# Kernel optimization log

Measured on AMD Instinct MI355X. Metric: run time of the kernel, lower is better.

## Reference

```python
import jax, jax.numpy as jnp
import numpy as np

N_NODES = 50000
IN_CH = 512
HID = 256
HEADS = 4
N_LAYERS = 2
LN_EPS = 1e-5


def _layer_norm(x, g, b):
    mu = jnp.mean(x, axis=-1, keepdims=True)
    var = jnp.mean((x - mu) ** 2, axis=-1, keepdims=True)
    return (x - mu) * jax.lax.rsqrt(var + LN_EPS) * g + b


def _trans_conv(x, wq, bq, wk, bk, wv, bv):
    # x: [N, HID]; projections -> [N, HEADS, HID]
    N = x.shape[0]
    qs = (x @ wq + bq).reshape(N, HEADS, HID)
    ks = (x @ wk + bk).reshape(N, HEADS, HID)
    vs = (x @ wv + bv).reshape(N, HEADS, HID)
    # NOTE: global Frobenius norm, matching torch.norm(t, p=2)
    qs = qs / jnp.linalg.norm(qs)
    ks = ks / jnp.linalg.norm(ks)
    kvs = jnp.einsum('lhm,lhd->hmd', ks, vs)                 # [H, C, C]
    attn_num = jnp.einsum('nhm,hmd->nhd', qs, kvs) + N * vs  # [N, H, C]
    ks_sum = jnp.sum(ks, axis=0)                             # [H, C]
    denom = jnp.einsum('nhm,hm->nh', qs, ks_sum)[..., None] + N
    return jnp.mean(attn_num / denom, axis=1)                # [N, HID]


def setup_inputs() -> dict:
    key = jax.random.key(0)
    ks = jax.random.split(key, 32)
    s_in = 1.0 / np.sqrt(IN_CH)
    s_h = 1.0 / np.sqrt(HID)
    inp = {
        'x': jax.random.normal(ks[0], (N_NODES, IN_CH), jnp.float32),
        'fc_w': jax.random.uniform(ks[1], (IN_CH, HID), jnp.float32, -s_in, s_in),
        'fc_b': jax.random.uniform(ks[2], (HID,), jnp.float32, -s_in, s_in),
        'ln0_g': jnp.ones((HID,), jnp.float32),
        'ln0_b': jnp.zeros((HID,), jnp.float32),
    }
    for i in range(N_LAYERS):
        base = 3 + i * 8
        inp[f'wq{i}'] = jax.random.uniform(ks[base + 0], (HID, HID * HEADS), jnp.float32, -s_h, s_h)
        inp[f'bq{i}'] = jax.random.uniform(ks[base + 1], (HID * HEADS,), jnp.float32, -s_h, s_h)
        inp[f'wk{i}'] = jax.random.uniform(ks[base + 2], (HID, HID * HEADS), jnp.float32, -s_h, s_h)
        inp[f'bk{i}'] = jax.random.uniform(ks[base + 3], (HID * HEADS,), jnp.float32, -s_h, s_h)
        inp[f'wv{i}'] = jax.random.uniform(ks[base + 4], (HID, HID * HEADS), jnp.float32, -s_h, s_h)
        inp[f'bv{i}'] = jax.random.uniform(ks[base + 5], (HID * HEADS,), jnp.float32, -s_h, s_h)
        inp[f'ln{i + 1}_g'] = jnp.ones((HID,), jnp.float32)
        inp[f'ln{i + 1}_b'] = jnp.zeros((HID,), jnp.float32)
    return inp


def reference(x, fc_w, fc_b, ln0_g, ln0_b,
              wq0, bq0, wk0, bk0, wv0, bv0, ln1_g, ln1_b,
              wq1, bq1, wk1, bk1, wv1, bv1, ln2_g, ln2_b):
    # input FFN path (ffn is hard-coded True); dropout is identity in eval mode
    h = jax.nn.relu(_layer_norm(x @ fc_w + fc_b, ln0_g, ln0_b))
    layers = [(wq0, bq0, wk0, bk0, wv0, bv0, ln1_g, ln1_b),
              (wq1, bq1, wk1, bk1, wv1, bv1, ln2_g, ln2_b)]
    for (wq, bq, wk, bk, wv, bv, g, b) in layers:
        prev = h
        h = _trans_conv(h, wq, bq, wk, bk, wv, bv)
        h = (h + prev) / 2.0
        h = jax.nn.relu(_layer_norm(h, g, b))
    return h
```

## Files before the change

kernel.cpp:

```cpp
#include <hip/hip_runtime.h>

#define NN    50000
#define IN_CH 512
#define HID   256
#define PJ    1024
#define FN    50000.0f
#define KTP   50176
#define NCH   98
#define CHK   512

typedef __attribute__((ext_vector_type(4)))  float f32x4;
typedef __attribute__((ext_vector_type(16))) float f32x16;
typedef __attribute__((ext_vector_type(4)))  int   i32x4;
typedef __attribute__((ext_vector_type(8)))  unsigned short u16x8;

__device__ inline void mfma16(f32x4& c, i32x4 a, i32x4 b){
  asm("v_mfma_f32_16x16x32_bf16 %0, %1, %2, %0" : "+v"(c) : "v"(a), "v"(b));
}
__device__ inline void mfma32(f32x16& c, i32x4 a, i32x4 b){
  asm("v_mfma_f32_32x32x16_bf16 %0, %1, %2, %0" : "+v"(c) : "v"(a), "v"(b));
}

__device__ inline unsigned short f2bf(float f){
  unsigned int u = __builtin_bit_cast(unsigned int, f);
  unsigned int r = (u + 0x7fffu + ((u >> 16) & 1u)) >> 16;
  return (unsigned short)r;
}
__device__ inline float bf2f(unsigned short u){
  unsigned int x = ((unsigned int)u) << 16;
  return __builtin_bit_cast(float, x);
}

__device__ inline float wave_reduce(float v){
  #pragma unroll
  for(int o=32;o>0;o>>=1) v += __shfl_down(v,o,64);
  return v;
}
__device__ inline float block_reduce(float v, float* sh4){
  v = wave_reduce(v);
  int lane = threadIdx.x & 63, wv = threadIdx.x >> 6;
  if(lane==0) sh4[wv] = v;
  __syncthreads();
  float r = sh4[0]+sh4[1]+sh4[2]+sh4[3];
  __syncthreads();
  return r;
}

__global__ void wconv(const float* __restrict__ w, unsigned short* __restrict__ wt){
  int idx = blockIdx.x*256 + threadIdx.x;
  if(idx >= IN_CH*HID) return;
  int k = idx >> 8, n = idx & 255;
  wt[((size_t)(k>>6)*256 + n)*64 + (k&63)] = f2bf(w[idx]);
}

__global__ __launch_bounds__(512)
void ffn_gemm(const float* __restrict__ X, const unsigned short* __restrict__ FWT2,
              const float* __restrict__ bias, const float* __restrict__ g,
              const float* __restrict__ b2, unsigned short* __restrict__ hbo){
  __shared__ __align__(16) unsigned char smem[55296];
  unsigned short (*as)[72] = (unsigned short(*)[72])smem;
  unsigned short (*bs)[72] = (unsigned short(*)[72])(smem + 18432);
  int t = threadIdx.x;
  int bm = blockIdx.x*128;
  int w = t>>6, lane = t&63;
  int wr = w>>2, wc = w&3;
  f32x4 acc[4][4];
  #pragma unroll
  for(int i=0;i<4;i++)
    #pragma unroll
    for(int j=0;j<4;j++) acc[i][j] = (f32x4){0.f,0.f,0.f,0.f};

  for(int k0=0;k0<IN_CH;k0+=64){
    { int r = t>>2, q = t&3;
      const float* src = X + (size_t)(bm+r)*IN_CH + k0 + q*16;
      bool ok = (bm+r) < NN;
      #pragma unroll
      for(int i=0;i<4;i++){
        float4 v = ok ? *(const float4*)(src + i*4) : make_float4(0.f,0.f,0.f,0.f);
        ushort4 u; u.x=f2bf(v.x); u.y=f2bf(v.y); u.z=f2bf(v.z); u.w=f2bf(v.w);
        *(ushort4*)&as[r][q*16 + i*4] = u;
      }
    }
    { int n = t>>1, q = t&1;
      const unsigned short* src = FWT2 + (size_t)(k0>>6)*16384 + (size_t)t*32;
      #pragma unroll
      for(int i=0;i<4;i++)
        *(u16x8*)&bs[n][q*32 + i*8] = *(const u16x8*)(src + i*8);
    }
    __syncthreads();
    #pragma unroll
    for(int ks=0;ks<2;ks++){
      i32x4 af[4], bfv[4];
      #pragma unroll
      for(int i=0;i<4;i++) af[i]  = *(const i32x4*)&as[wr*64 + i*16 + (lane&15)][ks*32 + (lane>>4)*8];
      #pragma unroll
      for(int j=0;j<4;j++) bfv[j] = *(const i32x4*)&bs[wc*64 + j*16 + (lane&15)][ks*32 + (lane>>4)*8];
      #pragma unroll
      for(int i=0;i<4;i++)
        #pragma unroll
        for(int j=0;j<4;j++) mfma16(acc[i][j], af[i], bfv[j]);
    }
    __syncthreads();
  }
  int cb = wc*64;
  #pragma unroll
  for(int j=0;j<4;j++){
    float bb = bias[cb + j*16 + (lane&15)];
    #pragma unroll
    for(int i=0;i<4;i++)
      #pragma unroll
      for(int r=0;r<4;r++) acc[i][j][r] += bb;
  }
  float (*lnp)[4][2] = (float(*)[4][2])smem;
  float (*lnstat)[2] = (float(*)[2])(smem + 4096);
  #pragma unroll
  for(int i=0;i<4;i++)
    #pragma unroll
    for(int r=0;r<4;r++){
      float s=0.f, q=0.f;
      #pragma unroll
      for(int j=0;j<4;j++){ float a=acc[i][j][r]; s+=a; q+=a*a; }
      #pragma unroll
      for(int m=1;m<16;m<<=1){ s += __shfl_xor(s,m,64); q += __shfl_xor(q,m,64); }
      if((lane&15)==0){
        int row = wr*64 + i*16 + (lane>>4)*4 + r;
        lnp[row][wc][0]=s; lnp[row][wc][1]=q;
      }
    }
  __syncthreads();
  if(t<128){
    float s=0.f,q=0.f;
    #pragma unroll
    for(int c=0;c<4;c++){ s+=lnp[t][c][0]; q+=lnp[t][c][1]; }
    float mu = s*(1.f/HID);
    float var = q*(1.f/HID) - mu*mu;
    lnstat[t][0]=mu; lnstat[t][1]=rsqrtf(var+1e-5f);
  }
  __syncthreads();
  #pragma unroll
  for(int j=0;j<4;j++){
    int col = cb + j*16 + (lane&15);
    float gg = g[col], bb = b2[col];
    #pragma unroll
    for(int i=0;i<4;i++)
      #pragma unroll
      for(int r=0;r<4;r++){
        int row = wr*64 + i*16 + (lane>>4)*4 + r;
        int grow = bm + row;
        if(grow<NN){
          float y = fmaxf((acc[i][j][r]-lnstat[row][0])*lnstat[row][1]*gg + bb, 0.f);
          hbo[(size_t)grow*HID + col] = f2bf(y);
        }
      }
  }
}

__global__ void ln_relu2(const float* __restrict__ in, const float* __restrict__ g,
                         const float* __restrict__ b, unsigned short* __restrict__ outb,
                         float* __restrict__ outf, int M){
  int lane = threadIdx.x & 63, wv = threadIdx.x >> 6;
  int row = blockIdx.x*4 + wv;
  if(row>=M) return;
  const float* r = in + (size_t)row*HID;
  float v[4], sum=0.f, sq=0.f;
  #pragma unroll
  for(int j=0;j<4;j++){ v[j]=r[lane+j*64]; sum+=v[j]; sq+=v[j]*v[j]; }
  sum = wave_reduce(sum); sq = wave_reduce(sq);
  sum = __shfl(sum,0,64); sq = __shfl(sq,0,64);
  float mu = sum*(1.f/HID);
  float var = sq*(1.f/HID) - mu*mu;
  float rs = rsqrtf(var + 1e-5f);
  #pragma unroll
  for(int j=0;j<4;j++){ int c=lane+j*64;
    float y = fmaxf((v[j]-mu)*rs*g[c] + b[c], 0.f);
    if(outb) outb[(size_t)row*HID + c] = f2bf(y);
    if(outf) outf[(size_t)row*HID + c] = y;
  }
}

__global__ __launch_bounds__(256)
void transpose_h(const unsigned short* __restrict__ hb, unsigned short* __restrict__ ht){
  __shared__ unsigned short ts[64][72];
  int r0 = blockIdx.x*64, c0 = blockIdx.y*64;
  int t = threadIdx.x;
  { int r = t&63, q = t>>6;
    #pragma unroll
    for(int i=0;i<2;i++){
      int c = q*16 + i*8;
      u16x8 v = {0,0,0,0,0,0,0,0};
      if(r0+r < NN) v = *(const u16x8*)(hb + (size_t)(r0+r)*HID + c0 + c);
      *(u16x8*)&ts[r][c] = v;
    }
  }
  __syncthreads();
  { int c = t>>2, q = t&3;
    unsigned short tmp[16];
    #pragma unroll
    for(int i=0;i<16;i++) tmp[i] = ts[q*16+i][c];
    unsigned short* dst = ht + (size_t)(c0+c)*KTP + r0 + q*16;
    *(u16x8*)(dst)   = *(u16x8*)&tmp[0];
    *(u16x8*)(dst+8) = *(u16x8*)&tmp[8];
  }
}

__global__ __launch_bounds__(256)
void gram_mfma(const unsigned short* __restrict__ ht, float* __restrict__ gp){
  __shared__ unsigned short as[128][72], bs[128][72];
  int q = blockIdx.x, ch = blockIdx.y;
  int r0 = (q>>1)*128, c0 = (q&1)*128;
  int t = threadIdx.x, w=t>>6, lane=t&63;
  int wr=w>>1, wc=w&1;
  f32x4 acc[4][4];
  #pragma unroll
  for(int i=0;i<4;i++)
    #pragma unroll
    for(int j=0;j<4;j++) acc[i][j] = (f32x4){0.f,0.f,0.f,0.f};
  size_t kbase = (size_t)ch*CHK;
  for(int k0=0;k0<CHK;k0+=64){
    { int r = t>>1, h2 = t&1;
      const unsigned short* srcA = ht + (size_t)(r0+r)*KTP + kbase + k0 + h2*32;
      const unsigned short* srcB = ht + (size_t)(c0+r)*KTP + kbase + k0 + h2*32;
      #pragma unroll
      for(int i=0;i<4;i++) *(u16x8*)&as[r][h2*32+i*8] = *(const u16x8*)(srcA + i*8);
      #pragma unroll
      for(int i=0;i<4;i++) *(u16x8*)&bs[r][h2*32+i*8] = *(const u16x8*)(srcB + i*8);
    }
    __syncthreads();
    #pragma unroll
    for(int ks=0;ks<2;ks++){
      i32x4 af[4], bfv[4];
      #pragma unroll
      for(int i=0;i<4;i++) af[i]  = *(const i32x4*)&as[wr*64 + i*16 + (lane&15)][ks*32 + (lane>>4)*8];
      #pragma unroll
      for(int j=0;j<4;j++) bfv[j] = *(const i32x4*)&bs[wc*64 + j*16 + (lane&15)][ks*32 + (lane>>4)*8];
      #pragma unroll
      for(int i=0;i<4;i++)
        #pragma unroll
        for(int j=0;j<4;j++) mfma16(acc[i][j], af[i], bfv[j]);
    }
    __syncthreads();
  }
  float* dst = gp + ((size_t)q*NCH + ch)*16384;
  #pragma unroll
  for(int i=0;i<4;i++)
    #pragma unroll
    for(int j=0;j<4;j++)
      #pragma unroll
      for(int r=0;r<4;r++)
        dst[(wr*64+i*16+(lane>>4)*4+r)*128 + wc*64+j*16+(lane&15)] = acc[i][j][r];
}

__global__ void gram_reduce2(const float* __restrict__ gp, float* __restrict__ G){
  int q=blockIdx.x; int e = blockIdx.y*256 + threadIdx.x;
  const float* p = gp + (size_t)q*NCH*16384 + e;
  float s=0.f;
  for(int c=0;c<NCH;c++) s += p[(size_t)c*16384];
  int i = e>>7, j = e&127;
  int r0=(q>>1)*128, c0=(q&1)*128;
  G[(r0+i)*256 + c0+j] = s;
}

__global__ void rowsum_ht(const unsigned short* __restrict__ ht, float* __restrict__ svec){
  int row = blockIdx.x;
  const unsigned short* p = ht + (size_t)row*KTP;
  float s = 0.f;
  for(int i = threadIdx.x*8; i < KTP; i += 2048){
    u16x8 v = *(const u16x8*)(p + i);
    #pragma unroll
    for(int e=0;e<8;e++) s += bf2f(v[e]);
  }
  __shared__ float sh4[4];
  float tot = block_reduce(s, sh4);
  if(threadIdx.x==0) svec[row] = tot;
}

__global__ void gw_gemm3(const float* __restrict__ G, const float* __restrict__ Wq,
                         const float* __restrict__ Wk, const float* __restrict__ Wv,
                         float* __restrict__ gw){
  const float* B = blockIdx.z==0?Wq:(blockIdx.z==1?Wk:Wv);
  float* C = gw + (size_t)blockIdx.z*262144;
  __shared__ float As[64][33];
  __shared__ float Bs[32][64];
  int bm = blockIdx.x*64, bn = blockIdx.y*64;
  int t = threadIdx.x;
  int tn = t & 15, tm = t >> 4;
  float acc[4][4] = {};
  for(int k0=0;k0<HID;k0+=32){
    { int kk=t&31, rr=t>>5;
      #pragma unroll
      for(int p=0;p<8;p++){ int r=rr+p*8;
        As[r][kk] = G[(size_t)(bm+r)*HID + k0+kk]; } }
    { int nn=t&63, kr=t>>6;
      #pragma unroll
      for(int p=0;p<8;p++){ int k=kr+p*4;
        Bs[k][nn] = B[(size_t)(k0+k)*PJ + bn+nn]; } }
    __syncthreads();
    for(int k=0;k<32;k++){
      float a[4], b[4];
      #pragma unroll
      for(int i=0;i<4;i++) a[i]=As[tm*4+i][k];
      #pragma unroll
      for(int j=0;j<4;j++) b[j]=Bs[k][tn*4+j];
      #pragma unroll
      for(int i=0;i<4;i++)
        #pragma unroll
        for(int j=0;j<4;j++) acc[i][j] += a[i]*b[j];
    }
    __syncthreads();
  }
  #pragma unroll
  for(int i=0;i<4;i++)
    #pragma unroll
    for(int j=0;j<4;j++)
      C[(size_t)(bm+tm*4+i)*PJ + bn+tn*4+j] = acc[i][j];
}

__global__ void wt_s(const float* __restrict__ Wq, const float* __restrict__ Wk,
                     const float* __restrict__ Wv, const float* __restrict__ s,
                     float* __restrict__ avec){
  const float* Wsel = (blockIdx.x==0)?Wq:(blockIdx.x==1)?Wk:Wv;
  int col = blockIdx.y*256 + threadIdx.x;
  __shared__ float ss[256];
  ss[threadIdx.x]=s[threadIdx.x];
  __syncthreads();
  float acc=0.f;
  for(int i=0;i<256;i++) acc += Wsel[(size_t)i*PJ + col]*ss[i];
  avec[blockIdx.x*1024 + col]=acc;
}

__global__ void trace_partial(const float* __restrict__ Wq, const float* __restrict__ Wk,
                              const float* __restrict__ gw, float* __restrict__ trp){
  int which = blockIdx.x;
  const float* Wsel = which ? Wk : Wq;
  const float* GW = gw + (size_t)which*262144;
  int t=threadIdx.x;
  int base = blockIdx.y*4096 + t;
  float s=0.f;
  #pragma unroll
  for(int i=0;i<16;i++){ int idx=base+i*256; s += Wsel[idx]*GW[idx]; }
  __shared__ float sh4[4];
  float r = block_reduce(s, sh4);
  if(t==0) trp[which*64 + blockIdx.y] = r;
}

__global__ void finalize_scalars(const float* __restrict__ trp, const float* __restrict__ bq,
                                 const float* __restrict__ bk, const float* __restrict__ avec,
                                 float* __restrict__ ksum, float* __restrict__ scal){
  __shared__ float sh4[4];
  int t=threadIdx.x;
  float pq = (t<64)? trp[t]    : 0.f;
  float pk = (t<64)? trp[64+t] : 0.f;
  float bqaq=0.f,bkak=0.f,bq2=0.f,bk2=0.f;
  #pragma unroll
  for(int p=0;p<4;p++){ int jn=t+p*256;
    float qv=bq[jn], kv=bk[jn];
    bqaq += qv*avec[jn]; bkak += kv*avec[1024+jn];
    bq2 += qv*qv; bk2 += kv*kv; }
  float tq = block_reduce(pq, sh4);
  float tk = block_reduce(pk, sh4);
  float s1 = block_reduce(bqaq, sh4);
  float s2 = block_reduce(bkak, sh4);
  float s3 = block_reduce(bq2, sh4);
  float s4 = block_reduce(bk2, sh4);
  if(t==0){
    float q2 = tq + 2.f*s1 + FN*s3;
    float k2 = tk + 2.f*s2 + FN*s4;
    scal[0] = rsqrtf(q2)*rsqrtf(k2);
  }
  #pragma unroll
  for(int p=0;p<4;p++){ int jn=t+p*256; ksum[jn] = avec[1024+jn] + FN*bk[jn]; }
}

__global__ void kvs_k(const float* __restrict__ Wk, const float* __restrict__ GWv,
                      const float* __restrict__ avec, const float* __restrict__ bk,
                      const float* __restrict__ bv, float* __restrict__ kvs){
  int hh=blockIdx.x, tile=blockIdx.y;
  int m0=(tile>>2)*64, d0=(tile&3)*64;
  __shared__ float As[32][64], Bs[32][64];
  int t=threadIdx.x, tn=t&15, tm=t>>4;
  float acc[4][4]={};
  for(int k0=0;k0<256;k0+=32){
    int kr=t>>6, cc=t&63;
    #pragma unroll
    for(int p=0;p<8;p++){
      int k=kr+p*4;
      As[k][cc] = Wk [(size_t)(k0+k)*PJ + hh*256 + m0+cc];
      Bs[k][cc] = GWv[(size_t)(k0+k)*PJ + hh*256 + d0+cc];
    }
    __syncthreads();
    for(int k=0;k<32;k++){
      float a[4], b[4];
      #pragma unroll
      for(int i=0;i<4;i++) a[i]=As[k][tm*4+i];
      #pragma unroll
      for(int j=0;j<4;j++) b[j]=Bs[k][tn*4+j];
      #pragma unroll
      for(int i=0;i<4;i++)
        #pragma unroll
        for(int j=0;j<4;j++) acc[i][j] += a[i]*b[j];
    }
    __syncthreads();
  }
  const float* ak = avec+1024; const float* av = avec+2048;
  #pragma unroll
  for(int i=0;i<4;i++)
    #pragma unroll
    for(int j=0;j<4;j++){
      int m=m0+tm*4+i, d=d0+tn*4+j;
      float akm=ak[hh*256+m], bkm=bk[hh*256+m];
      float avd=av[hh*256+d], bvd=bv[hh*256+d];
      kvs[(size_t)hh*65536 + m*256 + d] = acc[i][j] + akm*bvd + bkm*avd + FN*bkm*bvd;
    }
}

__global__ void u_gemm(const float* __restrict__ Wq, const float* __restrict__ kvs,
                       const float* __restrict__ Wv, const float* __restrict__ scal,
                       unsigned short* __restrict__ Ut2){
  int hh=blockIdx.x, tile=blockIdx.y;
  int i0=(tile>>2)*64, d0=(tile&3)*64;
  __shared__ float As[64][33]; __shared__ float Bs[32][64];
  int t=threadIdx.x, tn=t&15, tm=t>>4;
  float acc[4][4]={};
  for(int k0=0;k0<256;k0+=32){
    { int kk=t&31, rr=t>>5;
      #pragma unroll
      for(int p=0;p<8;p++){ int r=rr+p*8;
        As[r][kk] = Wq[(size_t)(i0+r)*PJ + hh*256 + k0+kk]; } }
    { int kr=t>>6, cc=t&63;
      #pragma unroll
      for(int p=0;p<8;p++){ int k=kr+p*4;
        Bs[k][cc] = kvs[(size_t)hh*65536 + (k0+k)*256 + d0+cc]; } }
    __syncthreads();
    for(int k=0;k<32;k++){
      float a[4], b[4];
      #pragma unroll
      for(int i=0;i<4;i++) a[i]=As[tm*4+i][k];
      #pragma unroll
      for(int j=0;j<4;j++) b[j]=Bs[k][tn*4+j];
      #pragma unroll
      for(int i=0;i<4;i++)
        #pragma unroll
        for(int j=0;j<4;j++) acc[i][j] += a[i]*b[j];
    }
    __syncthreads();
  }
  float sc = scal[0];
  #pragma unroll
  for(int i=0;i<4;i++)
    #pragma unroll
    for(int j=0;j<4;j++){
      int ii=i0+tm*4+i, d=d0+tn*4+j;
      float val = sc*acc[i][j] + FN*Wv[(size_t)ii*PJ + hh*256 + d];
      Ut2[((size_t)(d>>6)*4 + (ii>>6))*16384 + ((size_t)hh*64 + (d&63))*64 + (ii&63)] = f2bf(val);
    }
}

__global__ void head_vecs(const float* __restrict__ Wq, const float* __restrict__ bq,
                          const float* __restrict__ bv, const float* __restrict__ kvs,
                          const float* __restrict__ ksum, const float* __restrict__ scal,
                          float* __restrict__ uvec, float* __restrict__ wvec,
                          float* __restrict__ cvec){
  int hh=blockIdx.x, t=threadIdx.x;
  float scale=scal[0];
  __shared__ float bqs[256], kss[256];
  __shared__ float sh4[4];
  bqs[t]=bq[hh*256+t]; kss[t]=ksum[hh*256+t];
  __syncthreads();
  float su=0.f;
  for(int m=0;m<256;m++) su += bqs[m]*kvs[(size_t)hh*65536 + m*256 + t];
  uvec[hh*256+t] = scale*su + FN*bv[hh*256+t];
  float sw=0.f;
  for(int m=0;m<256;m++) sw += Wq[(size_t)t*PJ + hh*256 + m]*kss[m];
  wvec[hh*256+t] = scale*sw;
  float pc = bqs[t]*kss[t];
  float total = block_reduce(pc, sh4);
  if(t==0) cvec[hh] = scale*total + FN;
}

__global__ void denom_k(const unsigned short* __restrict__ hb, const float* __restrict__ wvec,
                        const float* __restrict__ cvec, float* __restrict__ denom, int M){
  __shared__ float wvl[1024];
  for(int i=threadIdx.x;i<1024;i+=256) wvl[i]=wvec[i];
  __syncthreads();
  int lane=threadIdx.x&63, wv=threadIdx.x>>6;
  int row=blockIdx.x*4+wv;
  if(row>=M) return;
  ushort4 hv = *(const ushort4*)(hb + (size_t)row*HID + lane*4);
  float h0=bf2f(hv.x), h1=bf2f(hv.y), h2=bf2f(hv.z), h3=bf2f(hv.w);
  float p[4];
  #pragma unroll
  for(int hh=0;hh<4;hh++){
    const float* wl = wvl + hh*256 + lane*4;
    p[hh] = h0*wl[0] + h1*wl[1] + h2*wl[2] + h3*wl[3];
  }
  #pragma unroll
  for(int hh=0;hh<4;hh++) p[hh]=wave_reduce(p[hh]);
  if(lane==0){
    #pragma unroll
    for(int hh=0;hh<4;hh++) denom[(size_t)row*4+hh] = 1.0f/(p[hh]+cvec[hh]);
  }
}

__global__ __launch_bounds__(512,4)
void attn_mfma(const unsigned short* __restrict__ hb, const unsigned short* __restrict__ Ut2,
               const float* __restrict__ uvec, const float* __restrict__ rden,
               float* __restrict__ outp){
  __shared__ __align__(16) unsigned char smem[38912];
  unsigned short (*bs)[72] = (unsigned short(*)[72])smem;
  float (*red)[64] = (float(*)[64])smem;
  float (*rsh)[4]  = (float(*)[4])(smem + 36864);
  int bm = blockIdx.x*128;
  int st = blockIdx.y;
  int t = threadIdx.x, w = t>>6, lane = t&63;
  int wr = w>>1, wc = w&1;
  int nst = t>>1, koff = (t&1)*32;

  f32x16 acc[4];
  #pragma unroll
  for(int j=0;j<4;j++)
    #pragma unroll
    for(int e=0;e<16;e++) acc[j][e]=0.f;

  { int r = t>>2, h2 = t&3;
    rsh[r][h2] = (bm+r<NN) ? rden[(size_t)(bm+r)*4+h2] : 1.0f; }

  const unsigned short* tb0 = Ut2 + (size_t)st*4*16384;
  u16x8 breg[4];
  #pragma unroll
  for(int i=0;i<4;i++) breg[i] = *(const u16x8*)(tb0 + (size_t)t*32 + i*8);

  int arow = bm + wr*32 + (lane&31); if(arow >= NN) arow = NN-1;
  const unsigned short* ap = hb + (size_t)arow*HID + (lane>>5)*8;

  #pragma unroll
  for(int kb=0;kb<4;kb++){
    __syncthreads();
    #pragma unroll
    for(int i=0;i<4;i++) *(u16x8*)&bs[nst][koff + i*8] = breg[i];
    __syncthreads();
    if(kb<3){
      const unsigned short* tn2 = Ut2 + ((size_t)st*4 + kb+1)*16384;
      #pragma unroll
      for(int i=0;i<4;i++) breg[i] = *(const u16x8*)(tn2 + (size_t)t*32 + i*8);
    }
    i32x4 a[4];
    #pragma unroll
    for(int ks=0;ks<4;ks++) a[ks] = *(const i32x4*)(ap + kb*64 + ks*16);
    #pragma unroll
    for(int ks=0;ks<4;ks++){
      int kc = ks*16 + (lane>>5)*8;
      #pragma unroll
      for(int j=0;j<4;j++){
        i32x4 b = *(const i32x4*)&bs[wc*128 + j*32 + (lane&31)][kc];
        mfma32(acc[j], a[ks], b);
      }
    }
  }
  float uv[4];
  #pragma unroll
  for(int j=0;j<4;j++)
    uv[j] = uvec[(wc*2 + (j>>1))*256 + st*64 + (j&1)*32 + (lane&31)];
  __syncthreads();
  if(wc==1){
    #pragma unroll
    for(int r=0;r<16;r++){
      int row = wr*32 + (r&3) + ((r>>2)<<3) + ((lane>>5)<<2);
      float d0 = rsh[row][2], d1 = rsh[row][3];
      red[row][lane&31]      = (acc[0][r]+uv[0])*d0 + (acc[2][r]+uv[2])*d1;
      red[row][32+(lane&31)] = (acc[1][r]+uv[1])*d0 + (acc[3][r]+uv[3])*d1;
    }
  }
  __syncthreads();
  if(wc==0){
    #pragma unroll
    for(int r=0;r<16;r++){
      int row = wr*32 + (r&3) + ((r>>2)<<3) + ((lane>>5)<<2);
      int gr = bm + row;
      if(gr < NN){
        float d0 = rsh[row][0], d1 = rsh[row][1];
        float v0 = ((acc[0][r]+uv[0])*d0 + (acc[2][r]+uv[2])*d1 + red[row][lane&31])      * 0.25f;
        float v1 = ((acc[1][r]+uv[1])*d0 + (acc[3][r]+uv[3])*d1 + red[row][32+(lane&31)]) * 0.25f;
        const unsigned short* hres = hb + (size_t)gr*HID + st*64;
        float* dst = outp + (size_t)gr*HID + st*64;
        dst[lane&31]      = (v0 + bf2f(hres[lane&31])) * 0.5f;
        dst[32+(lane&31)] = (v1 + bf2f(hres[32+(lane&31)])) * 0.5f;
      }
    }
  }
}

extern "C" void kernel_launch(void* const* d_in, const int* in_sizes, int n_in,
                              void* d_out, int out_size, void* d_ws, size_t ws_size,
                              hipStream_t stream){
  const float* x    = (const float*)d_in[0];
  const float* fc_w = (const float*)d_in[1];
  const float* fc_b = (const float*)d_in[2];
  const float* ln0g = (const float*)d_in[3];
  const float* ln0b = (const float*)d_in[4];
  float* out = (float*)d_out;

  float* W = (float*)d_ws;
  size_t o=0;
  float* buf1 = W+o; o+=(size_t)NN*HID;
  unsigned short* hb   = (unsigned short*)(W+o); o+=(size_t)NN*HID/2;
  unsigned short* ht   = (unsigned short*)(W+o); o+=(size_t)HID*KTP/2;
  unsigned short* FWT2 = (unsigned short*)(W+o); o+=(size_t)8*16384/2 + 8;
  unsigned short* Ut2  = (unsigned short*)(W+o); o+=(size_t)16*16384/2 + 8;
  float* gramp= W+o; o+=(size_t)4*NCH*16384;
  float* G    = W+o; o+=65536;
  float* gw   = W+o; o+=3*262144;
  float* svec = W+o; o+=256;
  float* avec = W+o; o+=3072;
  float* trp  = W+o; o+=128;
  float* scal = W+o; o+=16;
  float* ksum = W+o; o+=1024;
  float* kvs  = W+o; o+=262144;
  float* uvec = W+o; o+=1024;
  float* wvec = W+o; o+=1024;
  float* cvec = W+o; o+=8;
  float* denB = W+o; o+=(size_t)NN*4;
  (void)ws_size; (void)in_sizes; (void)n_in; (void)out_size;

  dim3 blk(256);
  wconv<<<dim3(512),blk,0,stream>>>(fc_w, FWT2);
  ffn_gemm<<<dim3(391),dim3(512),0,stream>>>(x, FWT2, fc_b, ln0g, ln0b, hb);

  for(int L=0; L<2; L++){
    const float* wq = (const float*)d_in[5+L*8+0];
    const float* bq = (const float*)d_in[5+L*8+1];
    const float* wk = (const float*)d_in[5+L*8+2];
    const float* bk = (const float*)d_in[5+L*8+3];
    const float* wv = (const float*)d_in[5+L*8+4];
    const float* bv = (const float*)d_in[5+L*8+5];
    const float* lng= (const float*)d_in[5+L*8+6];
    const float* lnb= (const float*)d_in[5+L*8+7];

    transpose_h<<<dim3(784,4),blk,0,stream>>>(hb, ht);
    gram_mfma<<<dim3(4,NCH),blk,0,stream>>>(ht, gramp);
    gram_reduce2<<<dim3(4,64),blk,0,stream>>>(gramp, G);
    rowsum_ht<<<dim3(256),blk,0,stream>>>(ht, svec);
    gw_gemm3<<<dim3(4,16,3),blk,0,stream>>>(G, wq, wk, wv, gw);
    wt_s<<<dim3(3,4),blk,0,stream>>>(wq,wk,wv,svec,avec);
    trace_partial<<<dim3(2,64),blk,0,stream>>>(wq,wk,gw,trp);
    finalize_scalars<<<dim3(1),blk,0,stream>>>(trp,bq,bk,avec,ksum,scal);
    kvs_k<<<dim3(4,16),blk,0,stream>>>(wk, gw+2*262144, avec, bk, bv, kvs);
    u_gemm<<<dim3(4,16),blk,0,stream>>>(wq, kvs, wv, scal, Ut2);
    head_vecs<<<dim3(4),blk,0,stream>>>(wq,bq,bv,kvs,ksum,scal,uvec,wvec,cvec);
    denom_k<<<dim3(12500),blk,0,stream>>>(hb, wvec, cvec, denB, NN);
    attn_mfma<<<dim3(391,4),dim3(512),0,stream>>>(hb, Ut2, uvec, denB, buf1);
    ln_relu2<<<dim3(12500),blk,0,stream>>>(buf1, lng, lnb,
                                           L ? (unsigned short*)nullptr : hb,
                                           L ? out : (float*)nullptr, NN);
  }
}
```

Measured before the change: 520.0 us.

## Exploit Gram symmetry and register-prefetch FFN GEMM tiles

The Gram matrix H^T H is symmetric, so only three of the four 128x128 quadrants are computed and the off-diagonal block is mirrored during the reduction. This cuts the gram GEMM and reduction work and the partial-sum buffer by a quarter. Separately, the FFN GEMM now loads the next K-tile of X and the weights into registers while the current tile runs its MFMAs, so global latency overlaps with compute at the cost of extra registers.

```diff
diff --git a/kernel.cpp b/kernel.cpp
--- a/kernel.cpp
+++ b/kernel.cpp
@@ -70,24 +70,41 @@
     #pragma unroll
     for(int j=0;j<4;j++) acc[i][j] = (f32x4){0.f,0.f,0.f,0.f};
 
-  for(int k0=0;k0<IN_CH;k0+=64){
-    { int r = t>>2, q = t&3;
-      const float* src = X + (size_t)(bm+r)*IN_CH + k0 + q*16;
-      bool ok = (bm+r) < NN;
+  int ar = t>>2, aq = t&3;
+  bool aok = (bm+ar) < NN;
+  const float* xsrc = X + (size_t)(bm+ar)*IN_CH + aq*16;
+  ushort4 aregs[4];
+  u16x8 bregs[4];
+  #pragma unroll
+  for(int i=0;i<4;i++){
+    float4 v = aok ? *(const float4*)(xsrc + i*4) : make_float4(0.f,0.f,0.f,0.f);
+    ushort4 u; u.x=f2bf(v.x); u.y=f2bf(v.y); u.z=f2bf(v.z); u.w=f2bf(v.w);
+    aregs[i]=u;
+  }
+  #pragma unroll
+  for(int i=0;i<4;i++) bregs[i] = *(const u16x8*)(FWT2 + (size_t)t*32 + i*8);
+
+  for(int kb=0;kb<8;kb++){
+    __syncthreads();
+    #pragma unroll
+    for(int i=0;i<4;i++) *(ushort4*)&as[ar][aq*16 + i*4] = aregs[i];
+    { int n = t>>1, q = t&1;
+      #pragma unroll
+      for(int i=0;i<4;i++) *(u16x8*)&bs[n][q*32 + i*8] = bregs[i];
+    }
+    __syncthreads();
+    if(kb<7){
+      const float* xs2 = xsrc + (kb+1)*64;
       #pragma unroll
       for(int i=0;i<4;i++){
-        float4 v = ok ? *(const float4*)(src + i*4) : make_float4(0.f,0.f,0.f,0.f);
+        float4 v = aok ? *(const float4*)(xs2 + i*4) : make_float4(0.f,0.f,0.f,0.f);
         ushort4 u; u.x=f2bf(v.x); u.y=f2bf(v.y); u.z=f2bf(v.z); u.w=f2bf(v.w);
-        *(ushort4*)&as[r][q*16 + i*4] = u;
+        aregs[i]=u;
       }
-    }
-    { int n = t>>1, q = t&1;
-      const unsigned short* src = FWT2 + (size_t)(k0>>6)*16384 + (size_t)t*32;
-      #pragma unroll
-      for(int i=0;i<4;i++)
-        *(u16x8*)&bs[n][q*32 + i*8] = *(const u16x8*)(src + i*8);
-    }
-    __syncthreads();
+      const unsigned short* bsrc = FWT2 + (size_t)(kb+1)*16384 + (size_t)t*32;
+      #pragma unroll
+      for(int i=0;i<4;i++) bregs[i] = *(const u16x8*)(bsrc + i*8);
+    }
     #pragma unroll
     for(int ks=0;ks<2;ks++){
       i32x4 af[4], bfv[4];
@@ -100,8 +117,8 @@
         #pragma unroll
         for(int j=0;j<4;j++) mfma16(acc[i][j], af[i], bfv[j]);
     }
-    __syncthreads();
-  }
+  }
+  __syncthreads();
   int cb = wc*64;
   #pragma unroll
   for(int j=0;j<4;j++){
@@ -205,8 +222,9 @@
 
 __global__ __launch_bounds__(256)
 void gram_mfma(const unsigned short* __restrict__ ht, float* __restrict__ gp){
+  const int qmap[3] = {0,1,3};
+  int qi = blockIdx.x, q = qmap[qi], ch = blockIdx.y;
   __shared__ unsigned short as[128][72], bs[128][72];
-  int q = blockIdx.x, ch = blockIdx.y;
   int r0 = (q>>1)*128, c0 = (q&1)*128;
   int t = threadIdx.x, w=t>>6, lane=t&63;
   int wr=w>>1, wc=w&1;
@@ -240,7 +258,7 @@
     }
     __syncthreads();
   }
-  float* dst = gp + ((size_t)q*NCH + ch)*16384;
+  float* dst = gp + ((size_t)qi*NCH + ch)*16384;
   #pragma unroll
   for(int i=0;i<4;i++)
     #pragma unroll
@@ -251,13 +269,14 @@
 }
 
 __global__ void gram_reduce2(const float* __restrict__ gp, float* __restrict__ G){
-  int q=blockIdx.x; int e = blockIdx.y*256 + threadIdx.x;
-  const float* p = gp + (size_t)q*NCH*16384 + e;
+  int qi=blockIdx.x; int e = blockIdx.y*256 + threadIdx.x;
+  const float* p = gp + (size_t)qi*NCH*16384 + e;
   float s=0.f;
   for(int c=0;c<NCH;c++) s += p[(size_t)c*16384];
   int i = e>>7, j = e&127;
-  int r0=(q>>1)*128, c0=(q&1)*128;
+  int r0 = (qi==2)?128:0, c0 = (qi==0)?0:128;
   G[(r0+i)*256 + c0+j] = s;
+  if(qi==1) G[(c0+j)*256 + (r0+i)] = s;
 }
 
 __global__ void rowsum_ht(const unsigned short* __restrict__ ht, float* __restrict__ svec){
@@ -606,7 +625,7 @@
   unsigned short* ht   = (unsigned short*)(W+o); o+=(size_t)HID*KTP/2;
   unsigned short* FWT2 = (unsigned short*)(W+o); o+=(size_t)8*16384/2 + 8;
   unsigned short* Ut2  = (unsigned short*)(W+o); o+=(size_t)16*16384/2 + 8;
-  float* gramp= W+o; o+=(size_t)4*NCH*16384;
+  float* gramp= W+o; o+=(size_t)3*NCH*16384;
   float* G    = W+o; o+=65536;
   float* gw   = W+o; o+=3*262144;
   float* svec = W+o; o+=256;
@@ -636,8 +655,8 @@
     const float* lnb= (const float*)d_in[5+L*8+7];
 
     transpose_h<<<dim3(784,4),blk,0,stream>>>(hb, ht);
-    gram_mfma<<<dim3(4,NCH),blk,0,stream>>>(ht, gramp);
-    gram_reduce2<<<dim3(4,64),blk,0,stream>>>(gramp, G);
+    gram_mfma<<<dim3(3,NCH),blk,0,stream>>>(ht, gramp);
+    gram_reduce2<<<dim3(3,64),blk,0,stream>>>(gramp, G);
     rowsum_ht<<<dim3(256),blk,0,stream>>>(ht, svec);
     gw_gemm3<<<dim3(4,16,3),blk,0,stream>>>(G, wq, wk, wv, gw);
     wt_s<<<dim3(3,4),blk,0,stream>>>(wq,wk,wv,svec,avec);
```

New measurement: 510.1 us. About the same (-1.9%).
